# Kernel tuning notes

Measured on AMD Instinct MI355X. Metric: run time of the kernel, lower is better.

## Reference

```python
import jax, jax.numpy as jnp
import numpy as np
from jax.scipy.special import gammaln, xlogy

H, K, V = 8, 64, 192          # heads, key_size, value_size
F = 192                        # num_relative_position_features
LN2 = 0.6931471805599453


def positional_features(T):
    """Enformer positional basis: exp half-life, central mask, gamma pdf;
    non-symmetric -> concat [emb, sign(pos)*emb]. Returns [2T-1, F]."""
    n = F // 6                                  # basis per class per symmetry
    pos = jnp.arange(-(T - 1), T, dtype=jnp.float32)   # [2T-1]
    ap = jnp.abs(pos)[:, None]                  # [2T-1, 1]
    # exponential (min_half_life=3.0, seq_length=T)
    max_range = jnp.log(float(T)) / LN2
    half_life = 2.0 ** jnp.linspace(3.0, max_range, n)
    fe = jnp.exp(-LN2 / half_life * ap)
    # central mask
    widths = 2.0 ** jnp.arange(1, n + 1, dtype=jnp.float32) - 1.0
    fm = (widths > ap).astype(jnp.float32)
    # gamma (stddev=T/(2n), start_mean=T/n)
    stddev = T / (2.0 * n)
    mean = jnp.linspace(T / float(n), float(T), n)
    conc = (mean / stddev) ** 2
    rate = mean / stddev ** 2
    log_p = xlogy(conc - 1.0, ap) - rate * ap - (gammaln(conc) - conc * jnp.log(rate))
    prob = jnp.exp(log_p) + 1e-8
    fg = prob / jnp.max(prob)
    emb = jnp.concatenate([fe, fm, fg], axis=-1)               # [2T-1, F/2]
    emb = jnp.concatenate([emb, jnp.sign(pos)[:, None] * emb], axis=-1)  # [2T-1, F]
    return emb


def relative_shift(x):
    """TransformerXL relative shift. x: [B,H,T,2T-1] -> [B,H,T,T]."""
    b, h, t1, r = x.shape                       # r == 2*t1 - 1
    x = jnp.pad(x, ((0, 0), (0, 0), (0, 0), (1, 0)))  # [B,H,T,2T]
    x = x.reshape(b, h, r + 1, t1)[:, :, 1:, :]        # [B,H,2T-1,T]
    x = x.reshape(b, h, t1, r)
    return x[..., :t1]


def setup_inputs() -> dict:
    key = jax.random.key(0)
    ks = jax.random.split(key, 8)
    B, T, D = 2, 1536, 1536
    s = 0.02
    return {
        "x": jax.random.normal(ks[0], (B, T, D), jnp.float32),
        "Wq": jax.random.normal(ks[1], (D, H * K), jnp.float32) * s,
        "Wk": jax.random.normal(ks[2], (D, H * K), jnp.float32) * s,
        "Wv": jax.random.normal(ks[3], (D, H * V), jnp.float32) * s,
        "Wrk": jax.random.normal(ks[4], (F, H * K), jnp.float32) * s,
        "Wemb": jax.random.normal(ks[5], (H * V, D), jnp.float32) * s,
        "r_w_bias": jax.random.normal(ks[6], (1, H, 1, K), jnp.float32) * s,
        "r_r_bias": jax.random.normal(ks[7], (1, H, 1, K), jnp.float32) * s,
    }


def reference(x, Wq, Wk, Wv, Wrk, Wemb, r_w_bias, r_r_bias):
    B, T, D = x.shape
    q = (x @ Wq).reshape(B, T, H, K).transpose(0, 2, 1, 3)   # [B,H,T,K]
    k = (x @ Wk).reshape(B, T, H, K).transpose(0, 2, 1, 3)
    v = (x @ Wv).reshape(B, T, H, V).transpose(0, 2, 1, 3)   # [B,H,T,V]
    q = q * (K ** -0.5)                                       # scaling
    emb = positional_features(T)                              # [2T-1, F]
    r_k = (emb @ Wrk).reshape(2 * T - 1, H, K).transpose(1, 0, 2)  # [H,2T-1,K]
    content = jnp.einsum('bhqk,bhmk->bhqm', q + r_w_bias, k)       # [B,H,T,T]
    rel = jnp.einsum('bhqk,hmk->bhqm', q + r_r_bias, r_k)          # [B,H,T,2T-1]
    logits = content + relative_shift(rel)
    w = jax.nn.softmax(logits, axis=-1)
    out = jnp.einsum('bhqm,bhmv->bhqv', w, v)                      # [B,H,T,V]
    out = out.transpose(0, 2, 1, 3).reshape(B, T, H * V)
    return out @ Wemb
```

## Files before the change

### kernel.cpp

```cpp
#include <hip/hip_runtime.h>
#include <stdint.h>

#define DEVI __device__ __forceinline__

typedef short bf16x8 __attribute__((ext_vector_type(8)));
typedef float f32x4 __attribute__((ext_vector_type(4)));

#define PMAX 0.01867013f

DEVI float b2f(unsigned short u) {
  union { unsigned u32; float f; } x;
  x.u32 = ((unsigned)u) << 16;
  return x.f;
}
DEVI unsigned short f2b(float f) {
  union { float f32; unsigned u32; } x;
  x.f32 = f;
  unsigned u = x.u32;
  return (unsigned short)((u + 0x7FFFu + ((u >> 16) & 1u)) >> 16);
}

DEVI void gload16(const unsigned short* g, unsigned short* l) {
  __builtin_amdgcn_global_load_lds(
      (const __attribute__((address_space(1))) void*)g,
      (__attribute__((address_space(3))) void*)l, 16, 0, 0);
}

DEVI float gamma_prob(float ap, int i) {
  float mean = 48.f * (float)(i + 1);
  float conc = (mean / 24.f) * (mean / 24.f);
  float rate = mean / 576.f;
  if (ap == 0.f) return 1e-8f;
  float logp = (conc - 1.f) * logf(ap) - rate * ap - (lgammaf(conc) - conc * logf(rate));
  return expf(logp) + 1e-8f;
}

DEVI void dev_transpose(const float* srcf, const unsigned short* srcb, int src_ld,
                        unsigned short* dst, int dst_ld, int rows, int cols,
                        int bx, int by, unsigned short (*t)[33]) {
  int tx = threadIdx.x & 31, ty = threadIdx.x >> 5;
  int r0 = by * 32, c0 = bx * 32;
#pragma unroll
  for (int i = 0; i < 4; i++) {
    int r = r0 + ty + i * 8, cc = c0 + tx;
    if (r < rows && cc < cols)
      t[ty + i * 8][tx] = srcf ? f2b(srcf[(size_t)r * src_ld + cc])
                               : srcb[(size_t)r * src_ld + cc];
  }
  __syncthreads();
#pragma unroll
  for (int i = 0; i < 4; i++) {
    int dr = c0 + ty + i * 8, dc = r0 + tx;
    if (dr < cols && dc < rows) dst[(size_t)dr * dst_ld + dc] = t[tx][ty + i * 8];
  }
}

__global__ __launch_bounds__(256) void k_prep(
    const float* __restrict__ x, const float* __restrict__ Wq,
    const float* __restrict__ Wk, const float* __restrict__ Wv,
    const float* __restrict__ Wemb, const float* __restrict__ Wrk,
    unsigned short* __restrict__ xb, unsigned short* __restrict__ WqkvT,
    unsigned short* __restrict__ WembT, unsigned short* __restrict__ WrkT,
    unsigned short* __restrict__ emb) {
  __shared__ unsigned short t[32][33];
  int bid = blockIdx.x;
  if (bid < 4608) {
    int i = (bid * 256 + threadIdx.x) * 4;
    float4 v = *(const float4*)(x + i);
    ushort4 o;
    o.x = f2b(v.x); o.y = f2b(v.y); o.z = f2b(v.z); o.w = f2b(v.w);
    *(ushort4*)(xb + i) = o;
  } else if (bid < 5376) {
    int s = bid - 4608;
    dev_transpose(Wq, nullptr, 512, WqkvT, 1536, 1536, 512, s % 16, s / 16, t);
  } else if (bid < 6144) {
    int s = bid - 5376;
    dev_transpose(Wk, nullptr, 512, WqkvT + (size_t)512 * 1536, 1536, 1536, 512, s % 16, s / 16, t);
  } else if (bid < 8448) {
    int s = bid - 6144;
    dev_transpose(Wv, nullptr, 1536, WqkvT + (size_t)1024 * 1536, 1536, 1536, 1536, s % 48, s / 48, t);
  } else if (bid < 10752) {
    int s = bid - 8448;
    dev_transpose(Wemb, nullptr, 1536, WembT, 1536, 1536, 1536, s % 48, s / 48, t);
  } else if (bid < 10848) {
    int s = bid - 10752;
    dev_transpose(Wrk, nullptr, 512, WrkT, 192, 192, 512, s % 16, s / 16, t);
  } else {
    int idx = (bid - 10848) * 256 + threadIdx.x;
    if (idx < 3071 * 96) {
      int m = idx / 96, cc = idx % 96;
      float ap = fabsf((float)(m - 1535));
      float val;
      if (cc < 32) {
        float max_range = logf(1536.f) * 1.4426950408889634f;
        float l = 3.f + (float)cc * (max_range - 3.f) / 31.f;
        val = exp2f(-ap * exp2f(-l));
      } else if (cc < 64) {
        float width = exp2f((float)(cc - 31)) - 1.f;
        val = (width > ap) ? 1.f : 0.f;
      } else {
        val = gamma_prob(ap, cc - 64) / PMAX;
      }
      float sgn = (m > 1535) ? 1.f : ((m < 1535) ? -1.f : 0.f);
      emb[(size_t)m * 192 + cc] = f2b(val);
      emb[(size_t)m * 192 + 96 + cc] = f2b(sgn * val);
    }
  }
}

DEVI void dev_gemm(const unsigned short* __restrict__ A, const unsigned short* __restrict__ Bt,
                   unsigned short* Cb, float* Cf, int M, int N, int K,
                   int bx, int by, unsigned short* As, unsigned short* Bs) {
  int tid = threadIdx.x;
  int w = tid >> 6, L = tid & 63, g = L >> 4, c = L & 15;
  int m0 = by << 7, n0 = bx << 7;
  int wm = (w >> 1) << 6, wn = (w & 1) << 6;
  f32x4 acc[4][4];
#pragma unroll
  for (int i = 0; i < 4; i++)
#pragma unroll
    for (int j = 0; j < 4; j++) acc[i][j] = (f32x4){0.f, 0.f, 0.f, 0.f};
  int nkt = K >> 5;
  for (int kt = 0; kt < nkt; kt++) {
    int k0 = kt << 5;
#pragma unroll
    for (int i2 = 0; i2 < 2; i2++) {
      int cidx = tid + (i2 << 8);
      int row = cidx >> 2, kc = (cidx & 3) << 3;
      int ra = m0 + row;
      if (ra >= M) ra = M - 1;
      gload16(A + (size_t)ra * K + k0 + kc, As + cidx * 8);
      gload16(Bt + (size_t)(n0 + row) * K + k0 + kc, Bs + cidx * 8);
    }
    __syncthreads();
    bf16x8 af[4], bfr[4];
#pragma unroll
    for (int t = 0; t < 4; t++) af[t] = *(const bf16x8*)(As + (wm + t * 16 + c) * 32 + g * 8);
#pragma unroll
    for (int t = 0; t < 4; t++) bfr[t] = *(const bf16x8*)(Bs + (wn + t * 16 + c) * 32 + g * 8);
#pragma unroll
    for (int mt = 0; mt < 4; mt++)
#pragma unroll
      for (int nt = 0; nt < 4; nt++)
        acc[mt][nt] = __builtin_amdgcn_mfma_f32_16x16x32_bf16(af[mt], bfr[nt], acc[mt][nt], 0, 0, 0);
    __syncthreads();
  }
#pragma unroll
  for (int mt = 0; mt < 4; mt++)
#pragma unroll
    for (int nt = 0; nt < 4; nt++)
#pragma unroll
      for (int r = 0; r < 4; r++) {
        int rr = m0 + wm + mt * 16 + g * 4 + r;
        if (rr < M) {
          size_t o = (size_t)rr * N + n0 + wn + nt * 16 + c;
          if (Cf) Cf[o] = acc[mt][nt][r];
          else Cb[o] = f2b(acc[mt][nt][r]);
        }
      }
}

__global__ __launch_bounds__(256) void k_gemm(
    const unsigned short* __restrict__ A, const unsigned short* __restrict__ Bt,
    unsigned short* Cb, float* Cf, int M, int N, int K) {
  __shared__ unsigned short sm[8192];
  dev_gemm(A, Bt, Cb, Cf, M, N, K, blockIdx.x, blockIdx.y, sm, sm + 4096);
}

__global__ __launch_bounds__(256) void k_mid(
    const unsigned short* __restrict__ emb, const unsigned short* __restrict__ WrkT,
    unsigned short* __restrict__ rkb, const unsigned short* __restrict__ QKV,
    unsigned short* __restrict__ Vt) {
  __shared__ unsigned short sm[8192];
  int bid = blockIdx.x;
  if (bid < 96) {
    dev_gemm(emb, WrkT, rkb, nullptr, 3071, 512, 192, bid & 3, bid >> 2, sm, sm + 4096);
  } else {
    int tt = bid - 96;
    int which = tt / 2304;
    tt %= 2304;
    dev_transpose(nullptr, QKV + 1024 + (size_t)which * 1536 * 2560, 2560,
                  Vt + (size_t)which * 1536 * 1536, 1536, 1536, 1536,
                  tt % 48, tt / 48, (unsigned short (*)[33])sm);
  }
}

__global__ __launch_bounds__(256, 2) void k_attn(
    const unsigned short* __restrict__ QKV, const unsigned short* __restrict__ rk,
    const unsigned short* __restrict__ Vt, const float* __restrict__ rwb,
    const float* __restrict__ rrb, float* __restrict__ Opart,
    float* __restrict__ lpart) {
  __shared__ unsigned short lds[28672];
  const int tid = threadIdx.x;
  const int w = tid >> 6, L = tid & 63, g = L >> 4, c = L & 15;
  const int bid = blockIdx.x;
  const int h = bid & 7, b = (bid >> 3) & 1, kh = (bid >> 4) & 1;
  const int i0b = (bid >> 5) << 7;
  const int qp = i0b + w * 32;
  const int bh = b * 8 + h;
  const int c7s = (c & 7) << 3;

  const int lrow8 = L >> 3;
  const int lbo = (((L & 7) * 16) ^ ((lrow8 & 7) << 4));

  bf16x8 aqw[2][2], aqr[2][2];
#pragma unroll
  for (int qi = 0; qi < 2; qi++) {
    const unsigned short* qrow =
        QKV + (size_t)(b * 1536 + qp + qi * 16 + c) * 2560 + h * 64;
#pragma unroll
    for (int ks = 0; ks < 2; ks++) {
      union { bf16x8 v; unsigned short s[8]; } uw, ur;
#pragma unroll
      for (int j = 0; j < 8; j++) {
        int d = ks * 32 + g * 8 + j;
        float qv = b2f(qrow[d]) * 0.125f;
        uw.s[j] = f2b(qv + rwb[h * 64 + d]);
        ur.s[j] = f2b(qv + rrb[h * 64 + d]);
      }
      aqw[qi][ks] = uw.v;
      aqr[qi][ks] = ur.v;
    }
  }

  int baddr[4], bsel[4];
#pragma unroll
  for (int r = 0; r < 4; r++) {
    int u = c - (g * 4 + r) + 15;
    baddr[r] = (((g << 4) | (u & 15)) << 2);
    bsel[r] = (u >> 4) & 1;
  }

  f32x4 Ofr[8][3];
#pragma unroll
  for (int s = 0; s < 8; s++)
#pragma unroll
    for (int t = 0; t < 3; t++) Ofr[s][t] = (f32x4){0.f, 0.f, 0.f, 0.f};
  float lrow[2][4] = {{0.f, 0.f, 0.f, 0.f}, {0.f, 0.f, 0.f, 0.f}};

  const unsigned short* rkh = rk + h * 64;
  const size_t kgbase = (size_t)(b * 1536 + kh * 768) * 2560 + 512 + h * 64;
  const size_t vgbase = (size_t)(bh * 192) * 1536 + kh * 768;

  auto stageK = [&](int kt, int nb) {
#pragma unroll
    for (int i = 0; i < 2; i++) {
      int key = w * 16 + i * 8 + lrow8;
      const unsigned short* src =
          QKV + kgbase + (size_t)(kt * 64 + key) * 2560 + (lbo >> 1);
      gload16(src, lds + nb * 4096 + w * 1024 + i * 512);
    }
  };
  auto stageV = [&](int kt) {
#pragma unroll
    for (int i = 0; i < 6; i++) {
      int vd = w * 48 + i * 8 + lrow8;
      const unsigned short* src =
          Vt + vgbase + (size_t)vd * 1536 + kt * 64 + (lbo >> 1);
      gload16(src, lds + 8192 + w * 3072 + i * 512);
    }
  };

  stageK(0, 0);
  __syncthreads();

  for (int jt = 0; jt < 12; jt++) {
    const int cur = jt & 1;
    stageV(jt);
    if (jt < 11) stageK(jt + 1, cur ^ 1);

    const int j0g = kh * 768 + jt * 64;
    const int moff1 = j0g - (qp + 16) + 1520;
    const unsigned short* kb = lds + cur * 4096;

    f32x4 Sc[2][4];
#pragma unroll
    for (int nt = 0; nt < 4; nt++) {
      const int kro = (nt * 16 + c) * 64;
      bf16x8 kf0 = *(const bf16x8*)(kb + kro + ((g * 8) ^ c7s));
      bf16x8 kf1 = *(const bf16x8*)(kb + kro + ((32 + g * 8) ^ c7s));
      f32x4 z0 = (f32x4){0.f, 0.f, 0.f, 0.f};
      z0 = __builtin_amdgcn_mfma_f32_16x16x32_bf16(aqw[0][0], kf0, z0, 0, 0, 0);
      z0 = __builtin_amdgcn_mfma_f32_16x16x32_bf16(aqw[0][1], kf1, z0, 0, 0, 0);
      Sc[0][nt] = z0;
      f32x4 z1 = (f32x4){0.f, 0.f, 0.f, 0.f};
      z1 = __builtin_amdgcn_mfma_f32_16x16x32_bf16(aqw[1][0], kf0, z1, 0, 0, 0);
      z1 = __builtin_amdgcn_mfma_f32_16x16x32_bf16(aqw[1][1], kf1, z1, 0, 0, 0);
      Sc[1][nt] = z1;
    }

    float bandp0[4], bandp1[4];
    {
      int mg = moff1 + c;
      const unsigned short* rrow = rkh + (size_t)mg * 512;
      f32x4 z = (f32x4){0.f, 0.f, 0.f, 0.f};
      z = __builtin_amdgcn_mfma_f32_16x16x32_bf16(aqr[1][0], *(const bf16x8*)(rrow + g * 8), z, 0, 0, 0);
      z = __builtin_amdgcn_mfma_f32_16x16x32_bf16(aqr[1][1], *(const bf16x8*)(rrow + 32 + g * 8), z, 0, 0, 0);
#pragma unroll
      for (int r = 0; r < 4; r++)
        bandp1[r] = __int_as_float(__builtin_amdgcn_ds_bpermute(baddr[r], __float_as_int(z[r])));
    }
#pragma unroll
    for (int j = 1; j <= 5; j++) {
      int mg = moff1 + 16 * j + c;
      if (mg > 3070) mg = 3070;
      const unsigned short* rrow = rkh + (size_t)mg * 512;
      bf16x8 rf0 = *(const bf16x8*)(rrow + g * 8);
      bf16x8 rf1 = *(const bf16x8*)(rrow + 32 + g * 8);
      {
        f32x4 z = (f32x4){0.f, 0.f, 0.f, 0.f};
        z = __builtin_amdgcn_mfma_f32_16x16x32_bf16(aqr[0][0], rf0, z, 0, 0, 0);
        z = __builtin_amdgcn_mfma_f32_16x16x32_bf16(aqr[0][1], rf1, z, 0, 0, 0);
        if (j == 1) {
#pragma unroll
          for (int r = 0; r < 4; r++)
            bandp0[r] = __int_as_float(__builtin_amdgcn_ds_bpermute(baddr[r], __float_as_int(z[r])));
        } else {
          const int nt = j - 2;
#pragma unroll
          for (int r = 0; r < 4; r++) {
            float bandc = __int_as_float(__builtin_amdgcn_ds_bpermute(baddr[r], __float_as_int(z[r])));
            Sc[0][nt][r] += bsel[r] ? bandc : bandp0[r];
            bandp0[r] = bandc;
          }
        }
      }
      if (j <= 4) {
        f32x4 z = (f32x4){0.f, 0.f, 0.f, 0.f};
        z = __builtin_amdgcn_mfma_f32_16x16x32_bf16(aqr[1][0], rf0, z, 0, 0, 0);
        z = __builtin_amdgcn_mfma_f32_16x16x32_bf16(aqr[1][1], rf1, z, 0, 0, 0);
        const int nt = j - 1;
#pragma unroll
        for (int r = 0; r < 4; r++) {
          float bandc = __int_as_float(__builtin_amdgcn_ds_bpermute(baddr[r], __float_as_int(z[r])));
          Sc[1][nt][r] += bsel[r] ? bandc : bandp1[r];
          bandp1[r] = bandc;
        }
      }
    }

#pragma unroll
    for (int qi = 0; qi < 2; qi++) {
      unsigned short* slab = lds + 20480 + (2 * w + qi) * 1024;
#pragma unroll
      for (int nt = 0; nt < 4; nt++)
#pragma unroll
        for (int r = 0; r < 4; r++) {
          float p = __expf(Sc[qi][nt][r]);
          lrow[qi][r] += p;
          int q = g * 4 + r;
          slab[q * 64 + ((nt * 16 + c) ^ ((q & 7) << 3))] = f2b(p);
        }
    }

    __syncthreads();

    bf16x8 vf0[3], vf1[3];
#pragma unroll
    for (int vt = 0; vt < 3; vt++) {
      const int vro = 8192 + (w * 48 + vt * 16 + c) * 64;
      vf0[vt] = *(const bf16x8*)(lds + vro + ((g * 8) ^ c7s));
      vf1[vt] = *(const bf16x8*)(lds + vro + ((32 + g * 8) ^ c7s));
    }
    __builtin_amdgcn_s_setprio(1);
#pragma unroll
    for (int s = 0; s < 8; s++) {
      const unsigned short* slab = lds + 20480 + s * 1024;
      bf16x8 ap0 = *(const bf16x8*)(slab + c * 64 + ((g * 8) ^ c7s));
      bf16x8 ap1 = *(const bf16x8*)(slab + c * 64 + ((32 + g * 8) ^ c7s));
#pragma unroll
      for (int vt = 0; vt < 3; vt++) {
        Ofr[s][vt] = __builtin_amdgcn_mfma_f32_16x16x32_bf16(ap0, vf0[vt], Ofr[s][vt], 0, 0, 0);
        Ofr[s][vt] = __builtin_amdgcn_mfma_f32_16x16x32_bf16(ap1, vf1[vt], Ofr[s][vt], 0, 0, 0);
      }
    }
    __builtin_amdgcn_s_setprio(0);

    __syncthreads();
  }

#pragma unroll
  for (int qi = 0; qi < 2; qi++)
#pragma unroll
    for (int r = 0; r < 4; r++) {
      float s = lrow[qi][r];
      s += __shfl_xor(s, 1, 64);
      s += __shfl_xor(s, 2, 64);
      s += __shfl_xor(s, 4, 64);
      s += __shfl_xor(s, 8, 64);
      lrow[qi][r] = s;
    }
  if (c == 0) {
#pragma unroll
    for (int qi = 0; qi < 2; qi++)
#pragma unroll
      for (int r = 0; r < 4; r++)
        lpart[(size_t)((kh * 2 + b) * 8 + h) * 1536 + qp + qi * 16 + g * 4 + r] =
            lrow[qi][r];
  }
#pragma unroll
  for (int s = 0; s < 8; s++)
#pragma unroll
    for (int vt = 0; vt < 3; vt++)
#pragma unroll
      for (int r = 0; r < 4; r++)
        Opart[(size_t)(kh * 3072 + b * 1536 + i0b + s * 16 + g * 4 + r) * 1536 +
              h * 192 + w * 48 + vt * 16 + c] = Ofr[s][vt][r];
}

__global__ __launch_bounds__(256) void k_fin(
    const float* __restrict__ Op, const float* __restrict__ lp,
    unsigned short* __restrict__ O) {
  int idx = (blockIdx.x * 256 + threadIdx.x) * 8;
  int row = idx / 1536, c0 = idx % 1536;
  int b = row >> 11 ? 1 : (row >= 1536);
  b = row >= 1536;
  int q = row - b * 1536, hh = c0 / 192;
  float l = lp[(size_t)(b * 8 + hh) * 1536 + q] +
            lp[(size_t)((2 + b) * 8 + hh) * 1536 + q];
  float sc = 1.f / l;
  const float4* p0 = (const float4*)(Op + (size_t)row * 1536 + c0);
  const float4* p1 = (const float4*)(Op + (size_t)(3072 + row) * 1536 + c0);
#pragma unroll
  for (int half = 0; half < 2; half++) {
    float4 a = p0[half], bb = p1[half];
    ushort4 o;
    o.x = f2b((a.x + bb.x) * sc);
    o.y = f2b((a.y + bb.y) * sc);
    o.z = f2b((a.z + bb.z) * sc);
    o.w = f2b((a.w + bb.w) * sc);
    *(ushort4*)(O + (size_t)row * 1536 + c0 + half * 4) = o;
  }
}

extern "C" void kernel_launch(void* const* d_in, const int* in_sizes, int n_in,
                              void* d_out, int out_size, void* d_ws, size_t ws_size,
                              hipStream_t stream) {
  const float* x    = (const float*)d_in[0];
  const float* Wq   = (const float*)d_in[1];
  const float* Wk   = (const float*)d_in[2];
  const float* Wv   = (const float*)d_in[3];
  const float* Wrk  = (const float*)d_in[4];
  const float* Wemb = (const float*)d_in[5];
  const float* rwb  = (const float*)d_in[6];
  const float* rrb  = (const float*)d_in[7];

  char* ws = (char*)d_ws;
  size_t off = 0;
  auto alloc = [&](size_t bytes) -> void* {
    void* p = ws + off;
    off += (bytes + 255) & ~(size_t)255;
    return p;
  };
  unsigned short* xb    = (unsigned short*)alloc((size_t)3072 * 1536 * 2);
  unsigned short* WqkvT = (unsigned short*)alloc((size_t)2560 * 1536 * 2);
  unsigned short* WembT = (unsigned short*)alloc((size_t)1536 * 1536 * 2);
  unsigned short* WrkT  = (unsigned short*)alloc((size_t)512 * 192 * 2);
  unsigned short* QKV   = (unsigned short*)alloc((size_t)3072 * 2560 * 2);
  unsigned short* Vt    = (unsigned short*)alloc((size_t)2 * 1536 * 1536 * 2);
  unsigned short* emb   = (unsigned short*)alloc((size_t)3072 * 192 * 2);
  unsigned short* rkb   = (unsigned short*)alloc((size_t)3072 * 512 * 2);
  unsigned short* Obuf  = (unsigned short*)alloc((size_t)3072 * 1536 * 2);
  float*          Opart = (float*)alloc((size_t)2 * 3072 * 1536 * 4);
  float*          lpart = (float*)alloc((size_t)2 * 2 * 8 * 1536 * 4);

  k_prep<<<12000, 256, 0, stream>>>(x, Wq, Wk, Wv, Wemb, Wrk, xb, WqkvT, WembT, WrkT, emb);
  k_gemm<<<dim3(20, 24), 256, 0, stream>>>(xb, WqkvT, QKV, nullptr, 3072, 2560, 1536);
  k_mid<<<4704, 256, 0, stream>>>(emb, WrkT, rkb, QKV, Vt);
  k_attn<<<384, 256, 0, stream>>>(QKV, rkb, Vt, rwb, rrb, Opart, lpart);
  k_fin<<<2304, 256, 0, stream>>>(Opart, lpart, Obuf);
  k_gemm<<<dim3(12, 24), 256, 0, stream>>>(Obuf, WembT, nullptr, (float*)d_out, 3072, 1536, 1536);
}
```

Measured before the change: 278.0 us.

## Split attention keys four ways, single-buffer K, bf16 partials, exp2 softmax

The attention kernel now splits the key range into four chunks instead of two, doubling the grid to 768 blocks so more of the GPU is occupied. K staging drops from double to single buffering, moving the next-tile load after the barrier. This frees shared memory so three blocks can fit per CU. Partial outputs are stored as bf16 instead of fp32 to cut write and read traffic in the combine kernel, which now sums four partials. Queries are prescaled by log2(e) so exp2f can replace __expf. The risks are less overlap between K loads and compute, more partial-sum traffic, and a small precision loss from bf16 partials.

```diff
diff --git a/kernel.cpp b/kernel.cpp
--- a/kernel.cpp
+++ b/kernel.cpp
@@ -2,6 +2,7 @@
 #include <stdint.h>
 
 #define DEVI __device__ __forceinline__
+#define LOG2E 1.4426950408889634f
 
 typedef short bf16x8 __attribute__((ext_vector_type(8)));
 typedef float f32x4 __attribute__((ext_vector_type(4)));
@@ -185,17 +186,17 @@
   }
 }
 
-__global__ __launch_bounds__(256, 2) void k_attn(
+__global__ __launch_bounds__(256, 3) void k_attn(
     const unsigned short* __restrict__ QKV, const unsigned short* __restrict__ rk,
     const unsigned short* __restrict__ Vt, const float* __restrict__ rwb,
-    const float* __restrict__ rrb, float* __restrict__ Opart,
+    const float* __restrict__ rrb, unsigned short* __restrict__ Opart,
     float* __restrict__ lpart) {
-  __shared__ unsigned short lds[28672];
+  __shared__ unsigned short lds[24576];
   const int tid = threadIdx.x;
   const int w = tid >> 6, L = tid & 63, g = L >> 4, c = L & 15;
   const int bid = blockIdx.x;
-  const int h = bid & 7, b = (bid >> 3) & 1, kh = (bid >> 4) & 1;
-  const int i0b = (bid >> 5) << 7;
+  const int h = bid & 7, b = (bid >> 3) & 1, kh = (bid >> 4) & 3;
+  const int i0b = (bid >> 6) << 7;
   const int qp = i0b + w * 32;
   const int bh = b * 8 + h;
   const int c7s = (c & 7) << 3;
@@ -215,8 +216,8 @@
       for (int j = 0; j < 8; j++) {
         int d = ks * 32 + g * 8 + j;
         float qv = b2f(qrow[d]) * 0.125f;
-        uw.s[j] = f2b(qv + rwb[h * 64 + d]);
-        ur.s[j] = f2b(qv + rrb[h * 64 + d]);
+        uw.s[j] = f2b((qv + rwb[h * 64 + d]) * LOG2E);
+        ur.s[j] = f2b((qv + rrb[h * 64 + d]) * LOG2E);
       }
       aqw[qi][ks] = uw.v;
       aqr[qi][ks] = ur.v;
@@ -239,16 +240,16 @@
   float lrow[2][4] = {{0.f, 0.f, 0.f, 0.f}, {0.f, 0.f, 0.f, 0.f}};
 
   const unsigned short* rkh = rk + h * 64;
-  const size_t kgbase = (size_t)(b * 1536 + kh * 768) * 2560 + 512 + h * 64;
-  const size_t vgbase = (size_t)(bh * 192) * 1536 + kh * 768;
-
-  auto stageK = [&](int kt, int nb) {
+  const size_t kgbase = (size_t)(b * 1536 + kh * 384) * 2560 + 512 + h * 64;
+  const size_t vgbase = (size_t)(bh * 192) * 1536 + kh * 384;
+
+  auto stageK = [&](int kt) {
 #pragma unroll
     for (int i = 0; i < 2; i++) {
       int key = w * 16 + i * 8 + lrow8;
       const unsigned short* src =
           QKV + kgbase + (size_t)(kt * 64 + key) * 2560 + (lbo >> 1);
-      gload16(src, lds + nb * 4096 + w * 1024 + i * 512);
+      gload16(src, lds + w * 1024 + i * 512);
     }
   };
   auto stageV = [&](int kt) {
@@ -257,28 +258,25 @@
       int vd = w * 48 + i * 8 + lrow8;
       const unsigned short* src =
           Vt + vgbase + (size_t)vd * 1536 + kt * 64 + (lbo >> 1);
-      gload16(src, lds + 8192 + w * 3072 + i * 512);
+      gload16(src, lds + 4096 + w * 3072 + i * 512);
     }
   };
 
-  stageK(0, 0);
+  stageK(0);
   __syncthreads();
 
-  for (int jt = 0; jt < 12; jt++) {
-    const int cur = jt & 1;
+  for (int jt = 0; jt < 6; jt++) {
     stageV(jt);
-    if (jt < 11) stageK(jt + 1, cur ^ 1);
-
-    const int j0g = kh * 768 + jt * 64;
+
+    const int j0g = kh * 384 + jt * 64;
     const int moff1 = j0g - (qp + 16) + 1520;
-    const unsigned short* kb = lds + cur * 4096;
 
     f32x4 Sc[2][4];
 #pragma unroll
     for (int nt = 0; nt < 4; nt++) {
       const int kro = (nt * 16 + c) * 64;
-      bf16x8 kf0 = *(const bf16x8*)(kb + kro + ((g * 8) ^ c7s));
-      bf16x8 kf1 = *(const bf16x8*)(kb + kro + ((32 + g * 8) ^ c7s));
+      bf16x8 kf0 = *(const bf16x8*)(lds + kro + ((g * 8) ^ c7s));
+      bf16x8 kf1 = *(const bf16x8*)(lds + kro + ((32 + g * 8) ^ c7s));
       f32x4 z0 = (f32x4){0.f, 0.f, 0.f, 0.f};
       z0 = __builtin_amdgcn_mfma_f32_16x16x32_bf16(aqw[0][0], kf0, z0, 0, 0, 0);
       z0 = __builtin_amdgcn_mfma_f32_16x16x32_bf16(aqw[0][1], kf1, z0, 0, 0, 0);
@@ -341,12 +339,12 @@
 
 #pragma unroll
     for (int qi = 0; qi < 2; qi++) {
-      unsigned short* slab = lds + 20480 + (2 * w + qi) * 1024;
+      unsigned short* slab = lds + 16384 + (2 * w + qi) * 1024;
 #pragma unroll
       for (int nt = 0; nt < 4; nt++)
 #pragma unroll
         for (int r = 0; r < 4; r++) {
-          float p = __expf(Sc[qi][nt][r]);
+          float p = exp2f(Sc[qi][nt][r]);
           lrow[qi][r] += p;
           int q = g * 4 + r;
           slab[q * 64 + ((nt * 16 + c) ^ ((q & 7) << 3))] = f2b(p);
@@ -355,17 +353,19 @@
 
     __syncthreads();
 
+    if (jt < 5) stageK(jt + 1);
+
     bf16x8 vf0[3], vf1[3];
 #pragma unroll
     for (int vt = 0; vt < 3; vt++) {
-      const int vro = 8192 + (w * 48 + vt * 16 + c) * 64;
+      const int vro = 4096 + (w * 48 + vt * 16 + c) * 64;
       vf0[vt] = *(const bf16x8*)(lds + vro + ((g * 8) ^ c7s));
       vf1[vt] = *(const bf16x8*)(lds + vro + ((32 + g * 8) ^ c7s));
     }
     __builtin_amdgcn_s_setprio(1);
 #pragma unroll
     for (int s = 0; s < 8; s++) {
-      const unsigned short* slab = lds + 20480 + s * 1024;
+      const unsigned short* slab = lds + 16384 + s * 1024;
       bf16x8 ap0 = *(const bf16x8*)(slab + c * 64 + ((g * 8) ^ c7s));
       bf16x8 ap1 = *(const bf16x8*)(slab + c * 64 + ((32 + g * 8) ^ c7s));
 #pragma unroll
@@ -405,30 +405,41 @@
 #pragma unroll
       for (int r = 0; r < 4; r++)
         Opart[(size_t)(kh * 3072 + b * 1536 + i0b + s * 16 + g * 4 + r) * 1536 +
-              h * 192 + w * 48 + vt * 16 + c] = Ofr[s][vt][r];
+              h * 192 + w * 48 + vt * 16 + c] = f2b(Ofr[s][vt][r]);
 }
 
 __global__ __launch_bounds__(256) void k_fin(
-    const float* __restrict__ Op, const float* __restrict__ lp,
+    const unsigned short* __restrict__ Op, const float* __restrict__ lp,
     unsigned short* __restrict__ O) {
   int idx = (blockIdx.x * 256 + threadIdx.x) * 8;
   int row = idx / 1536, c0 = idx % 1536;
-  int b = row >> 11 ? 1 : (row >= 1536);
-  b = row >= 1536;
+  int b = row >= 1536;
   int q = row - b * 1536, hh = c0 / 192;
-  float l = lp[(size_t)(b * 8 + hh) * 1536 + q] +
-            lp[(size_t)((2 + b) * 8 + hh) * 1536 + q];
+  float l = 0.f;
+#pragma unroll
+  for (int kh = 0; kh < 4; kh++)
+    l += lp[(size_t)((kh * 2 + b) * 8 + hh) * 1536 + q];
   float sc = 1.f / l;
-  const float4* p0 = (const float4*)(Op + (size_t)row * 1536 + c0);
-  const float4* p1 = (const float4*)(Op + (size_t)(3072 + row) * 1536 + c0);
+  float acc[8] = {0.f, 0.f, 0.f, 0.f, 0.f, 0.f, 0.f, 0.f};
+#pragma unroll
+  for (int kh = 0; kh < 4; kh++) {
+    const ushort4* p = (const ushort4*)(Op + (size_t)(kh * 3072 + row) * 1536 + c0);
+#pragma unroll
+    for (int half = 0; half < 2; half++) {
+      ushort4 a = p[half];
+      acc[half * 4 + 0] += b2f(a.x);
+      acc[half * 4 + 1] += b2f(a.y);
+      acc[half * 4 + 2] += b2f(a.z);
+      acc[half * 4 + 3] += b2f(a.w);
+    }
+  }
 #pragma unroll
   for (int half = 0; half < 2; half++) {
-    float4 a = p0[half], bb = p1[half];
     ushort4 o;
-    o.x = f2b((a.x + bb.x) * sc);
-    o.y = f2b((a.y + bb.y) * sc);
-    o.z = f2b((a.z + bb.z) * sc);
-    o.w = f2b((a.w + bb.w) * sc);
+    o.x = f2b(acc[half * 4 + 0] * sc);
+    o.y = f2b(acc[half * 4 + 1] * sc);
+    o.z = f2b(acc[half * 4 + 2] * sc);
+    o.w = f2b(acc[half * 4 + 3] * sc);
     *(ushort4*)(O + (size_t)row * 1536 + c0 + half * 4) = o;
   }
 }
@@ -461,13 +472,13 @@
   unsigned short* emb   = (unsigned short*)alloc((size_t)3072 * 192 * 2);
   unsigned short* rkb   = (unsigned short*)alloc((size_t)3072 * 512 * 2);
   unsigned short* Obuf  = (unsigned short*)alloc((size_t)3072 * 1536 * 2);
-  float*          Opart = (float*)alloc((size_t)2 * 3072 * 1536 * 4);
-  float*          lpart = (float*)alloc((size_t)2 * 2 * 8 * 1536 * 4);
+  unsigned short* Opart = (unsigned short*)alloc((size_t)4 * 3072 * 1536 * 2);
+  float*          lpart = (float*)alloc((size_t)4 * 2 * 8 * 1536 * 4);
 
   k_prep<<<12000, 256, 0, stream>>>(x, Wq, Wk, Wv, Wemb, Wrk, xb, WqkvT, WembT, WrkT, emb);
   k_gemm<<<dim3(20, 24), 256, 0, stream>>>(xb, WqkvT, QKV, nullptr, 3072, 2560, 1536);
   k_mid<<<4704, 256, 0, stream>>>(emb, WrkT, rkb, QKV, Vt);
-  k_attn<<<384, 256, 0, stream>>>(QKV, rkb, Vt, rwb, rrb, Opart, lpart);
+  k_attn<<<768, 256, 0, stream>>>(QKV, rkb, Vt, rwb, rrb, Opart, lpart);
   k_fin<<<2304, 256, 0, stream>>>(Opart, lpart, Obuf);
   k_gemm<<<dim3(12, 24), 256, 0, stream>>>(Obuf, WembT, nullptr, (float*)d_out, 3072, 1536, 1536);
 }
```

After: 340.7 us. 22.6% more time.
